# Kernel optimization log

Hardware: AMD Instinct MI355X
Metric: run time of the kernel (lower is better)

## Reference

```python
import jax, jax.numpy as jnp
import numpy as np

NEG_SLOPE = 0.2
EPS = 1e-16


def _gat_layer(x, src, dst, W, a_src, a_dst, b, n_nodes):
    # x: [N, Fin], W: [Fout, Fin]; src/dst: [E'] (self-loops already appended)
    h = x @ W.T                              # [N, Fout]
    alpha_s = h @ a_src                      # [N] per-source score
    alpha_d = h @ a_dst                      # [N] per-dest score
    e = jax.nn.leaky_relu(alpha_s[src] + alpha_d[dst], NEG_SLOPE)  # [E']
    # segment softmax over destination nodes (PyG softmax semantics)
    m = jax.ops.segment_max(e, dst, num_segments=n_nodes)          # [N]
    ex = jnp.exp(e - m[dst])                                       # [E']
    s = jax.ops.segment_sum(ex, dst, num_segments=n_nodes)         # [N]
    alpha = ex / (s[dst] + EPS)                                    # [E']
    out = jax.ops.segment_sum(alpha[:, None] * h[src], dst, num_segments=n_nodes)
    return out + b, alpha


def setup_inputs() -> dict:
    key = jax.random.key(0)
    ks = jax.random.split(key, 14)
    N, E, F_IN, H1, H2, F_OUT = 50000, 800000, 128, 64, 64, 32
    sc = 0.1
    return {
        "x": jax.random.normal(ks[0], (N, F_IN), dtype=jnp.float32),
        "edge_index": jax.random.randint(ks[1], (2, E), 0, N, dtype=jnp.int64),
        "W1": jax.random.normal(ks[2], (H1, F_IN), dtype=jnp.float32) * sc,
        "a_src1": jax.random.normal(ks[3], (H1,), dtype=jnp.float32) * sc,
        "a_dst1": jax.random.normal(ks[4], (H1,), dtype=jnp.float32) * sc,
        "b1": jnp.zeros((H1,), dtype=jnp.float32),
        "W2": jax.random.normal(ks[5], (H2, H1), dtype=jnp.float32) * sc,
        "a_src2": jax.random.normal(ks[6], (H2,), dtype=jnp.float32) * sc,
        "a_dst2": jax.random.normal(ks[7], (H2,), dtype=jnp.float32) * sc,
        "b2": jnp.zeros((H2,), dtype=jnp.float32),
        "W3": jax.random.normal(ks[8], (F_OUT, H2), dtype=jnp.float32) * sc,
        "a_src3": jax.random.normal(ks[9], (F_OUT,), dtype=jnp.float32) * sc,
        "a_dst3": jax.random.normal(ks[10], (F_OUT,), dtype=jnp.float32) * sc,
        "b3": jnp.zeros((F_OUT,), dtype=jnp.float32),
    }


def reference(x, edge_index, W1, a_src1, a_dst1, b1, W2, a_src2, a_dst2, b2, W3, a_src3, a_dst3, b3):
    N = x.shape[0]
    loops = jnp.arange(N, dtype=edge_index.dtype)
    src = jnp.concatenate([edge_index[0], loops])  # add_self_loops=True
    dst = jnp.concatenate([edge_index[1], loops])

    h, alpha1 = _gat_layer(x, src, dst, W1, a_src1, a_dst1, b1, N)
    h = jax.nn.relu(h)
    h, _ = _gat_layer(h, src, dst, W2, a_src2, a_dst2, b2, N)
    h = jax.nn.relu(h)
    out, _ = _gat_layer(h, src, dst, W3, a_src3, a_dst3, b3, N)
    # att_tuple = (edge_index with self loops, attention coefficients of layer 1)
    return (jnp.stack([src, dst]), alpha1, out)
```

## Files before the change

### kernel.cpp

```cpp
#include <hip/hip_runtime.h>
#include <hip/hip_bf16.h>
#include <math.h>

#define NEG_SLOPE 0.2f
#define GAT_EPS 1e-16f

constexpr int NN = 50000;
constexpr int NE = 800000;
constexpr int EP = NE + NN;
constexpr int NB = (NN + 255) / 256;

constexpr int PB  = 128;
constexpr int PT  = 1024;
constexpr int CH  = (EP + PB - 1) / PB;
constexpr int NCH = 4;
constexpr int BPC = PB / NCH;

__device__ inline void edge_sd(const int* __restrict__ ei, int i, int& s, int& d) {
    if (i < NE) { s = ei[i]; d = ei[NE + i]; }
    else        { s = d = i - NE; }
}

__device__ inline float bflo(unsigned int h) { return __uint_as_float(h << 16); }
__device__ inline float bfhi(unsigned int h) { return __uint_as_float(h & 0xffff0000u); }

__global__ __launch_bounds__(PT) void k_p1_hist(const int* __restrict__ ei,
                                                float* __restrict__ out0,
                                                unsigned char* __restrict__ hist,
                                                unsigned char* __restrict__ rank8) {
    __shared__ unsigned int sh[NN / 4];
    int b = blockIdx.x, t = threadIdx.x;
    for (int w = t; w < NN / 4; w += PT) sh[w] = 0u;
    __syncthreads();
    int i0 = b * CH;
    int iend = i0 + CH; if (iend > EP) iend = EP;
    for (int i = i0 + t; i < iend; i += PT) {
        int s, d; edge_sd(ei, i, s, d);
        __builtin_nontemporal_store((float)s, &out0[i]);
        __builtin_nontemporal_store((float)d, &out0[EP + i]);
        int sft = (d & 3) * 8;
        unsigned int old = atomicAdd(&sh[d >> 2], 1u << sft);
        __builtin_nontemporal_store((unsigned char)(old >> sft), &rank8[i]);
    }
    __syncthreads();
    unsigned int* hw = (unsigned int*)(hist + (size_t)b * NN);
    for (int w = t; w < NN / 4; w += PT) hw[w] = sh[w];
}

__global__ __launch_bounds__(256) void k_p2s1(unsigned char* __restrict__ hist,
                                              unsigned char* __restrict__ chunkoff,
                                              int* __restrict__ rowptr,
                                              int* __restrict__ bsum) {
    __shared__ int sh[256];
    int t = threadIdx.x;
    int n = blockIdx.x * 256 + t;
    int v = 0;
    if (n < NN) {
        unsigned int runs[NCH];
#pragma unroll
        for (int c = 0; c < NCH; ++c) {
            size_t base = (size_t)(c * BPC) * NN + n;
            unsigned int vv[BPC];
#pragma unroll
            for (int b = 0; b < BPC; ++b) vv[b] = hist[base + (size_t)b * NN];
            unsigned int run = 0;
#pragma unroll
            for (int b = 0; b < BPC; ++b) { unsigned int x = vv[b]; vv[b] = run; run += x; }
#pragma unroll
            for (int b = 0; b < BPC; ++b) hist[base + (size_t)b * NN] = (unsigned char)vv[b];
            runs[c] = run;
        }
        unsigned int o1 = runs[0], o2 = o1 + runs[1], o3 = o2 + runs[2];
        *(unsigned int*)&chunkoff[(size_t)n * 4] = (o1 << 8) | (o2 << 16) | (o3 << 24);
        v = (int)(o3 + runs[3]);
    }
    sh[t] = v; __syncthreads();
    for (int off = 1; off < 256; off <<= 1) {
        int x = (t >= off) ? sh[t - off] : 0;
        __syncthreads();
        sh[t] += x;
        __syncthreads();
    }
    if (n < NN) rowptr[n] = sh[t] - v;
    if (t == 255) bsum[blockIdx.x] = sh[255];
}

__global__ __launch_bounds__(256) void k_s23(int* __restrict__ rowptr,
                                             const int* __restrict__ bsum) {
    __shared__ int sh[256];
    int t = threadIdx.x;
    int v = (t < NB) ? bsum[t] : 0;
    sh[t] = v; __syncthreads();
    for (int off = 1; off < 256; off <<= 1) {
        int x = (t >= off) ? sh[t - off] : 0;
        __syncthreads();
        sh[t] += x;
        __syncthreads();
    }
    int blk = blockIdx.x;
    int off = (blk == 0) ? 0 : sh[blk - 1];
    int n = blk * 256 + t;
    if (n < NN) rowptr[n] += off;
    if (n == 0) rowptr[NN] = EP;
}

__global__ __launch_bounds__(256) void k_fill(const int* __restrict__ ei,
                                              const unsigned char* __restrict__ rank8,
                                              const unsigned char* __restrict__ hist,
                                              const unsigned char* __restrict__ chunkoff,
                                              const int* __restrict__ rowptr,
                                              unsigned short* __restrict__ col) {
    int i = blockIdx.x * 256 + threadIdx.x;
    if (i >= EP) return;
    int b = i / CH;
    int c = b / BPC;
    int s, d; edge_sd(ei, i, s, d);
    int pos = rowptr[d] + (int)chunkoff[d * 4 + c] + (int)hist[(size_t)b * NN + d]
            + (int)rank8[i];
    col[pos] = (unsigned short)s;
}

__global__ void k_alpha_out(const int* __restrict__ ei, const float* __restrict__ as_,
                            const float* __restrict__ ad_, const float* __restrict__ inv,
                            float* __restrict__ out_alpha) {
    int i = blockIdx.x * blockDim.x + threadIdx.x;
    if (i >= EP) return;
    int s, d; edge_sd(ei, i, s, d);
    float v = as_[s] + ad_[d];
    v = v > 0.f ? v : NEG_SLOPE * v;
    __builtin_nontemporal_store(__expf(v) * inv[d], &out_alpha[i]);
}

struct alignas(8) bh4 { __hip_bfloat16 a, b, c, d; };

__device__ inline void fma4(float4& acc, float x, const float4& w) {
    acc.x = fmaf(x, w.x, acc.x);
    acc.y = fmaf(x, w.y, acc.y);
    acc.z = fmaf(x, w.z, acc.z);
    acc.w = fmaf(x, w.w, acc.w);
}

template <int FIN, int FOUT, int NPB>
__global__ __launch_bounds__(256) void k_gemm_t(const float* __restrict__ in,
                                                const float* __restrict__ W,
                                                const float* __restrict__ avs,
                                                const float* __restrict__ avd,
                                                __hip_bfloat16* __restrict__ H,
                                                float* __restrict__ as_,
                                                float* __restrict__ ad_, int n) {
    constexpr int TF = FOUT / 4;
    constexpr int XS = FIN + 4;
    constexpr int WS = FOUT + 4;
    __shared__ float sX[NPB * XS];
    __shared__ float sWt[FIN * WS];
    int tid = threadIdx.x;
    for (int idx = tid; idx < FIN * FOUT; idx += 256) {
        int f = idx % FOUT, k = idx / FOUT;
        sWt[k * WS + f] = W[f * FIN + k];
    }
    int nb = blockIdx.x * NPB;
    for (int idx = tid; idx < NPB * (FIN / 4); idx += 256) {
        int node = idx / (FIN / 4), kq = idx % (FIN / 4);
        int g = nb + node;
        float4 v = make_float4(0.f, 0.f, 0.f, 0.f);
        if (g < n) v = *(const float4*)&in[(size_t)g * FIN + kq * 4];
        *(float4*)&sX[node * XS + kq * 4] = v;
    }
    __syncthreads();

    int fq = tid % TF, ng = tid / TF;
    int n0 = ng * 4;
    float4 acc0 = make_float4(0.f, 0.f, 0.f, 0.f);
    float4 acc1 = acc0, acc2 = acc0, acc3 = acc0;
    for (int k = 0; k < FIN; k += 4) {
        float4 w0 = *(const float4*)&sWt[(k + 0) * WS + fq * 4];
        float4 w1 = *(const float4*)&sWt[(k + 1) * WS + fq * 4];
        float4 w2 = *(const float4*)&sWt[(k + 2) * WS + fq * 4];
        float4 w3 = *(const float4*)&sWt[(k + 3) * WS + fq * 4];
        float4 x0 = *(const float4*)&sX[(n0 + 0) * XS + k];
        float4 x1 = *(const float4*)&sX[(n0 + 1) * XS + k];
        float4 x2 = *(const float4*)&sX[(n0 + 2) * XS + k];
        float4 x3 = *(const float4*)&sX[(n0 + 3) * XS + k];
        fma4(acc0, x0.x, w0); fma4(acc0, x0.y, w1); fma4(acc0, x0.z, w2); fma4(acc0, x0.w, w3);
        fma4(acc1, x1.x, w0); fma4(acc1, x1.y, w1); fma4(acc1, x1.z, w2); fma4(acc1, x1.w, w3);
        fma4(acc2, x2.x, w0); fma4(acc2, x2.y, w1); fma4(acc2, x2.z, w2); fma4(acc2, x2.w, w3);
        fma4(acc3, x3.x, w0); fma4(acc3, x3.y, w1); fma4(acc3, x3.z, w2); fma4(acc3, x3.w, w3);
    }
    float4 accs[4] = {acc0, acc1, acc2, acc3};
    float4 vs4 = *(const float4*)&avs[fq * 4];
    float4 vd4 = *(const float4*)&avd[fq * 4];
#pragma unroll
    for (int j = 0; j < 4; ++j) {
        int g = nb + n0 + j;
        float ps = accs[j].x * vs4.x + accs[j].y * vs4.y + accs[j].z * vs4.z + accs[j].w * vs4.w;
        float pd = accs[j].x * vd4.x + accs[j].y * vd4.y + accs[j].z * vd4.z + accs[j].w * vd4.w;
#pragma unroll
        for (int off = TF / 2; off; off >>= 1) {
            ps += __shfl_down(ps, off, TF);
            pd += __shfl_down(pd, off, TF);
        }
        if (g < n) {
            if (fq == 0) { as_[g] = ps; ad_[g] = pd; }
            bh4 o;
            o.a = __float2bfloat16(accs[j].x);
            o.b = __float2bfloat16(accs[j].y);
            o.c = __float2bfloat16(accs[j].z);
            o.d = __float2bfloat16(accs[j].w);
            *(bh4*)&H[(size_t)g * FOUT + fq * 4] = o;
        }
    }
}

template <int FOUT, bool RELU, bool WRITE_INV>
__global__ __launch_bounds__(256) void k_attn_grp(
    const int* __restrict__ rowptr, const unsigned short* __restrict__ col,
    const float* __restrict__ as_, const float* __restrict__ ad_,
    const __hip_bfloat16* __restrict__ H, const float* __restrict__ bias,
    float* __restrict__ outp, float* __restrict__ inv_out) {
    constexpr int L = (FOUT == 64) ? 16 : 8;
    constexpr int GPW = 64 / L;
    int tid = blockIdx.x * 256 + threadIdx.x;
    int wid = tid >> 6;
    int lane = threadIdx.x & 63;
    int grp = lane / L;
    int gl  = lane & (L - 1);
    int node = wid * GPW + grp;
    if (node >= NN) return;

    int start = rowptr[node], end = rowptr[node + 1];
    float adv = ad_[node];
    const uint2* __restrict__ H4 = (const uint2*)H;
    int base = lane & ~(L - 1);

    float sloc = 0.f;
    float4 acc = make_float4(0.f, 0.f, 0.f, 0.f);
    for (int c = start; c < end; c += 8) {
        int e = c + gl;
        float p = 0.f;
        int sc = 0;
        if (gl < 8 && e < end) {
            sc = (int)col[e];
            float v = as_[sc] + adv;
            v = v > 0.f ? v : NEG_SLOPE * v;
            p = __expf(v);
        }
        sloc += p;
        int cnt = end - c; if (cnt > 8) cnt = 8;
        float pp[8]; int ss[8]; uint2 hh[8];
#pragma unroll
        for (int k = 0; k < 8; ++k) {
            pp[k] = __shfl(p, base + k);
            ss[k] = __shfl(sc, base + k);
        }
#pragma unroll
        for (int k = 0; k < 8; ++k) {
            hh[k] = make_uint2(0u, 0u);
            if (k < cnt) hh[k] = H4[(size_t)ss[k] * L + gl];
        }
#pragma unroll
        for (int k = 0; k < 8; ++k) {
            acc.x = fmaf(pp[k], bflo(hh[k].x), acc.x);
            acc.y = fmaf(pp[k], bfhi(hh[k].x), acc.y);
            acc.z = fmaf(pp[k], bflo(hh[k].y), acc.z);
            acc.w = fmaf(pp[k], bfhi(hh[k].y), acc.w);
        }
    }
#pragma unroll
    for (int off = L / 2; off; off >>= 1) sloc += __shfl_xor(sloc, off);
    float inv = 1.f / (sloc + GAT_EPS);
    if (WRITE_INV && gl == 0) inv_out[node] = inv;

    float4 bb = *(const float4*)&bias[gl * 4];
    float o0 = bb.x + acc.x * inv;
    float o1 = bb.y + acc.y * inv;
    float o2 = bb.z + acc.z * inv;
    float o3 = bb.w + acc.w * inv;
    if (RELU) {
        o0 = fmaxf(o0, 0.f); o1 = fmaxf(o1, 0.f);
        o2 = fmaxf(o2, 0.f); o3 = fmaxf(o3, 0.f);
    }
    *(float4*)&outp[(size_t)node * FOUT + gl * 4] = make_float4(o0, o1, o2, o3);
}

extern "C" void kernel_launch(void* const* d_in, const int* in_sizes, int n_in,
                              void* d_out, int out_size, void* d_ws, size_t ws_size,
                              hipStream_t stream) {
    const float* x  = (const float*)d_in[0];
    const int*   ei = (const int*)d_in[1];
    const float* W1 = (const float*)d_in[2];
    const float* as1 = (const float*)d_in[3];
    const float* ad1 = (const float*)d_in[4];
    const float* b1 = (const float*)d_in[5];
    const float* W2 = (const float*)d_in[6];
    const float* as2 = (const float*)d_in[7];
    const float* ad2 = (const float*)d_in[8];
    const float* b2 = (const float*)d_in[9];
    const float* W3 = (const float*)d_in[10];
    const float* as3 = (const float*)d_in[11];
    const float* ad3 = (const float*)d_in[12];
    const float* b3 = (const float*)d_in[13];

    float* out = (float*)d_out;
    float* out_edges = out;
    float* out_alpha = out + 2 * EP;
    float* out_final = out + 3 * EP;

    char* w = (char*)d_ws;
    size_t o = 0;
    auto alloc = [&](size_t bytes) { void* p = w + o; o = (o + bytes + 15) & ~15ull; return p; };
    float* as_ = (float*)alloc((size_t)NN * 4);
    float* ad_ = (float*)alloc((size_t)NN * 4);
    float* inv = (float*)alloc((size_t)NN * 4);
    __hip_bfloat16* H = (__hip_bfloat16*)alloc((size_t)NN * 64 * 2);
    int* rowptr = (int*)alloc((size_t)(NN + 1) * 4);
    unsigned char* rank8 = (unsigned char*)alloc((size_t)EP);
    unsigned short* col  = (unsigned short*)alloc((size_t)EP * 2);
    unsigned char* chunkoff = (unsigned char*)alloc((size_t)NN * 4);
    int* bsum = (int*)alloc(1024);

    const size_t aggBytes  = (size_t)NN * 64 * 4;
    const size_t histBytes = (size_t)PB * NN;
    float* agg = (ws_size >= o + aggBytes)
        ? (float*)(w + o)
        : (float*)d_in[0];
    unsigned char* hist = (ws_size >= o + aggBytes + histBytes)
        ? (unsigned char*)(w + o + aggBytes)
        : (unsigned char*)out_final;

    k_p1_hist<<<PB, PT, 0, stream>>>(ei, out_edges, hist, rank8);
    k_p2s1<<<NB, 256, 0, stream>>>(hist, chunkoff, rowptr, bsum);
    k_s23<<<NB, 256, 0, stream>>>(rowptr, bsum);
    k_fill<<<(EP + 255) / 256, 256, 0, stream>>>(ei, rank8, hist, chunkoff, rowptr, col);

    const int nblk64 = (NN + 15) / 16;
    const int nblk32 = (NN + 31) / 32;

    k_gemm_t<128, 64, 64><<<(NN + 63) / 64, 256, 0, stream>>>(x, W1, as1, ad1, H, as_, ad_, NN);
    k_attn_grp<64, true, true><<<nblk64, 256, 0, stream>>>(rowptr, col, as_, ad_, H, b1,
                                                           agg, inv);
    k_alpha_out<<<(EP + 255) / 256, 256, 0, stream>>>(ei, as_, ad_, inv, out_alpha);

    k_gemm_t<64, 64, 64><<<(NN + 63) / 64, 256, 0, stream>>>(agg, W2, as2, ad2, H, as_, ad_, NN);
    k_attn_grp<64, true, false><<<nblk64, 256, 0, stream>>>(rowptr, col, as_, ad_, H, b2,
                                                            agg, nullptr);

    k_gemm_t<64, 32, 128><<<(NN + 127) / 128, 256, 0, stream>>>(agg, W3, as3, ad3, H, as_, ad_,
                                                                NN);
    k_attn_grp<32, false, false><<<nblk32, 256, 0, stream>>>(rowptr, col, as_, ad_, H, b3,
                                                             out_final, nullptr);
}
```

Baseline: 273.1 us.

## Fuse attention aggregation with next-layer GEMM and fold rowptr scan into fill

Attention aggregation for layers 1 and 2 now also applies bias and ReLU, stages the result in shared memory and multiplies by the next layer's weight matrix in the same kernel. It emits bf16 features and attention scores directly, which removes the fp32 intermediate round-trip and two GEMM launches. The second-level prefix scan is folded into the fill kernel, with each block recomputing the block-sum scan redundantly. Separate buffers per layer avoid read/write hazards, and the aggregation drops the max-subtraction in the softmax, as the earlier code already appears to do.

```diff
diff --git a/kernel.cpp b/kernel.cpp
--- a/kernel.cpp
+++ b/kernel.cpp
@@ -85,39 +85,37 @@
     if (t == 255) bsum[blockIdx.x] = sh[255];
 }
 
-__global__ __launch_bounds__(256) void k_s23(int* __restrict__ rowptr,
-                                             const int* __restrict__ bsum) {
-    __shared__ int sh[256];
-    int t = threadIdx.x;
-    int v = (t < NB) ? bsum[t] : 0;
-    sh[t] = v; __syncthreads();
-    for (int off = 1; off < 256; off <<= 1) {
-        int x = (t >= off) ? sh[t - off] : 0;
-        __syncthreads();
-        sh[t] += x;
-        __syncthreads();
-    }
-    int blk = blockIdx.x;
-    int off = (blk == 0) ? 0 : sh[blk - 1];
-    int n = blk * 256 + t;
-    if (n < NN) rowptr[n] += off;
-    if (n == 0) rowptr[NN] = EP;
-}
-
 __global__ __launch_bounds__(256) void k_fill(const int* __restrict__ ei,
                                               const unsigned char* __restrict__ rank8,
                                               const unsigned char* __restrict__ hist,
                                               const unsigned char* __restrict__ chunkoff,
                                               const int* __restrict__ rowptr,
-                                              unsigned short* __restrict__ col) {
-    int i = blockIdx.x * 256 + threadIdx.x;
-    if (i >= EP) return;
-    int b = i / CH;
-    int c = b / BPC;
-    int s, d; edge_sd(ei, i, s, d);
-    int pos = rowptr[d] + (int)chunkoff[d * 4 + c] + (int)hist[(size_t)b * NN + d]
-            + (int)rank8[i];
-    col[pos] = (unsigned short)s;
+                                              const int* __restrict__ bsum,
+                                              unsigned short* __restrict__ col,
+                                              int* __restrict__ rowptrF) {
+    __shared__ int sb[256];
+    int t = threadIdx.x;
+    int v = (t < NB) ? bsum[t] : 0;
+    sb[t] = v; __syncthreads();
+    for (int off = 1; off < 256; off <<= 1) {
+        int x = (t >= off) ? sb[t - off] : 0;
+        __syncthreads();
+        sb[t] += x;
+        __syncthreads();
+    }
+    sb[t] -= v;
+    __syncthreads();
+    int i = blockIdx.x * 256 + t;
+    if (i < EP) {
+        int b = i / CH;
+        int c = b / BPC;
+        int s, d; edge_sd(ei, i, s, d);
+        int pos = rowptr[d] + sb[d >> 8] + (int)chunkoff[d * 4 + c]
+                + (int)hist[(size_t)b * NN + d] + (int)rank8[i];
+        col[pos] = (unsigned short)s;
+    }
+    if (i < NN) rowptrF[i] = rowptr[i] + sb[i >> 8];
+    if (i == 0) rowptrF[NN] = EP;
 }
 
 __global__ void k_alpha_out(const int* __restrict__ ei, const float* __restrict__ as_,
@@ -132,6 +130,7 @@
 }
 
 struct alignas(8) bh4 { __hip_bfloat16 a, b, c, d; };
+struct alignas(4) bh2 { __hip_bfloat16 a, b; };
 
 __device__ inline void fma4(float4& acc, float x, const float4& w) {
     acc.x = fmaf(x, w.x, acc.x);
@@ -211,6 +210,135 @@
     }
 }
 
+template <int GOUT, bool WRITE_INV>
+__global__ __launch_bounds__(256) void k_attn_fg(
+    const int* __restrict__ rowptr, const unsigned short* __restrict__ col,
+    const float* __restrict__ as_, const float* __restrict__ ad_,
+    const __hip_bfloat16* __restrict__ H, const float* __restrict__ bias,
+    const float* __restrict__ Wn,
+    const float* __restrict__ avs, const float* __restrict__ avd,
+    __hip_bfloat16* __restrict__ Hout,
+    float* __restrict__ as_out, float* __restrict__ ad_out,
+    float* __restrict__ inv_out) {
+    constexpr int NPB = 16;
+    __shared__ float sW[64][GOUT + 2];
+    __shared__ float sA[NPB][68];
+    int tid = threadIdx.x;
+    for (int idx = tid; idx < 64 * GOUT; idx += 256) {
+        int f = idx % GOUT, k = idx / GOUT;
+        sW[k][f] = Wn[f * 64 + k];
+    }
+
+    int lane = tid & 63;
+    int grp = lane >> 4, gl = lane & 15;
+    int lnode = (tid >> 6) * 4 + grp;
+    int node = blockIdx.x * NPB + lnode;
+    int base = lane & ~15;
+
+    if (node < NN) {
+        int start = rowptr[node], end = rowptr[node + 1];
+        float adv = ad_[node];
+        const uint2* __restrict__ H4 = (const uint2*)H;
+        float sloc = 0.f;
+        float4 acc = make_float4(0.f, 0.f, 0.f, 0.f);
+        for (int c = start; c < end; c += 8) {
+            int e = c + gl;
+            float p = 0.f;
+            int sc = 0;
+            if (gl < 8 && e < end) {
+                sc = (int)col[e];
+                float v = as_[sc] + adv;
+                v = v > 0.f ? v : NEG_SLOPE * v;
+                p = __expf(v);
+            }
+            sloc += p;
+            int cnt = end - c; if (cnt > 8) cnt = 8;
+            float pp[8]; int ss[8]; uint2 hh[8];
+#pragma unroll
+            for (int k = 0; k < 8; ++k) {
+                pp[k] = __shfl(p, base + k);
+                ss[k] = __shfl(sc, base + k);
+            }
+#pragma unroll
+            for (int k = 0; k < 8; ++k) {
+                hh[k] = make_uint2(0u, 0u);
+                if (k < cnt) hh[k] = H4[(size_t)ss[k] * 16 + gl];
+            }
+#pragma unroll
+            for (int k = 0; k < 8; ++k) {
+                acc.x = fmaf(pp[k], bflo(hh[k].x), acc.x);
+                acc.y = fmaf(pp[k], bfhi(hh[k].x), acc.y);
+                acc.z = fmaf(pp[k], bflo(hh[k].y), acc.z);
+                acc.w = fmaf(pp[k], bfhi(hh[k].y), acc.w);
+            }
+        }
+#pragma unroll
+        for (int off = 8; off; off >>= 1) sloc += __shfl_xor(sloc, off);
+        float inv = 1.f / (sloc + GAT_EPS);
+        if (WRITE_INV && gl == 0) inv_out[node] = inv;
+
+        float4 bb = *(const float4*)&bias[gl * 4];
+        sA[lnode][gl * 4 + 0] = fmaxf(bb.x + acc.x * inv, 0.f);
+        sA[lnode][gl * 4 + 1] = fmaxf(bb.y + acc.y * inv, 0.f);
+        sA[lnode][gl * 4 + 2] = fmaxf(bb.z + acc.z * inv, 0.f);
+        sA[lnode][gl * 4 + 3] = fmaxf(bb.w + acc.w * inv, 0.f);
+    }
+    __syncthreads();
+
+    int ng = tid >> 4, fq = tid & 15;
+    int gnode = blockIdx.x * NPB + ng;
+    if (gnode >= NN) return;
+    if (GOUT == 64) {
+        float4 a = make_float4(0.f, 0.f, 0.f, 0.f);
+#pragma unroll 8
+        for (int k = 0; k < 64; ++k) {
+            float xk = sA[ng][k];
+            const float* wr = &sW[k][fq * 4];
+            a.x = fmaf(xk, wr[0], a.x);
+            a.y = fmaf(xk, wr[1], a.y);
+            a.z = fmaf(xk, wr[2], a.z);
+            a.w = fmaf(xk, wr[3], a.w);
+        }
+        float4 vs = *(const float4*)&avs[fq * 4];
+        float4 vd = *(const float4*)&avd[fq * 4];
+        float ps = a.x * vs.x + a.y * vs.y + a.z * vs.z + a.w * vs.w;
+        float pd = a.x * vd.x + a.y * vd.y + a.z * vd.z + a.w * vd.w;
+#pragma unroll
+        for (int off = 8; off; off >>= 1) {
+            ps += __shfl_xor(ps, off);
+            pd += __shfl_xor(pd, off);
+        }
+        if (fq == 0) { as_out[gnode] = ps; ad_out[gnode] = pd; }
+        bh4 o;
+        o.a = __float2bfloat16(a.x);
+        o.b = __float2bfloat16(a.y);
+        o.c = __float2bfloat16(a.z);
+        o.d = __float2bfloat16(a.w);
+        *(bh4*)&Hout[(size_t)gnode * 64 + fq * 4] = o;
+    } else {
+        float ax = 0.f, ay = 0.f;
+#pragma unroll 8
+        for (int k = 0; k < 64; ++k) {
+            float xk = sA[ng][k];
+            const float* wr = &sW[k][fq * 2];
+            ax = fmaf(xk, wr[0], ax);
+            ay = fmaf(xk, wr[1], ay);
+        }
+        float ps = ax * avs[fq * 2] + ay * avs[fq * 2 + 1];
+        float pd = ax * avd[fq * 2] + ay * avd[fq * 2 + 1];
+#pragma unroll
+        for (int off = 8; off; off >>= 1) {
+            ps += __shfl_xor(ps, off);
+            pd += __shfl_xor(pd, off);
+        }
+        if (fq == 0) { as_out[gnode] = ps; ad_out[gnode] = pd; }
+        bh2 o;
+        o.a = __float2bfloat16(ax);
+        o.b = __float2bfloat16(ay);
+        *(bh2*)&Hout[(size_t)gnode * 32 + fq * 2] = o;
+    }
+}
+
 template <int FOUT, bool RELU, bool WRITE_INV>
 __global__ __launch_bounds__(256) void k_attn_grp(
     const int* __restrict__ rowptr, const unsigned short* __restrict__ col,
@@ -308,44 +436,44 @@
     char* w = (char*)d_ws;
     size_t o = 0;
     auto alloc = [&](size_t bytes) { void* p = w + o; o = (o + bytes + 15) & ~15ull; return p; };
-    float* as_ = (float*)alloc((size_t)NN * 4);
-    float* ad_ = (float*)alloc((size_t)NN * 4);
+    float* asA = (float*)alloc((size_t)NN * 4);
+    float* adA = (float*)alloc((size_t)NN * 4);
+    float* asB = (float*)alloc((size_t)NN * 4);
+    float* adB = (float*)alloc((size_t)NN * 4);
+    float* asC = (float*)alloc((size_t)NN * 4);
+    float* adC = (float*)alloc((size_t)NN * 4);
     float* inv = (float*)alloc((size_t)NN * 4);
-    __hip_bfloat16* H = (__hip_bfloat16*)alloc((size_t)NN * 64 * 2);
-    int* rowptr = (int*)alloc((size_t)(NN + 1) * 4);
+    __hip_bfloat16* H1 = (__hip_bfloat16*)alloc((size_t)NN * 64 * 2);
+    __hip_bfloat16* H2 = (__hip_bfloat16*)alloc((size_t)NN * 64 * 2);
+    __hip_bfloat16* H3 = (__hip_bfloat16*)alloc((size_t)NN * 32 * 2);
+    int* rowptr  = (int*)alloc((size_t)(NN + 1) * 4);
+    int* rowptrF = (int*)alloc((size_t)(NN + 1) * 4);
     unsigned char* rank8 = (unsigned char*)alloc((size_t)EP);
     unsigned short* col  = (unsigned short*)alloc((size_t)EP * 2);
     unsigned char* chunkoff = (unsigned char*)alloc((size_t)NN * 4);
     int* bsum = (int*)alloc(1024);
 
-    const size_t aggBytes  = (size_t)NN * 64 * 4;
     const size_t histBytes = (size_t)PB * NN;
-    float* agg = (ws_size >= o + aggBytes)
-        ? (float*)(w + o)
-        : (float*)d_in[0];
-    unsigned char* hist = (ws_size >= o + aggBytes + histBytes)
-        ? (unsigned char*)(w + o + aggBytes)
+    unsigned char* hist = (ws_size >= o + histBytes)
+        ? (unsigned char*)(w + o)
         : (unsigned char*)out_final;
 
     k_p1_hist<<<PB, PT, 0, stream>>>(ei, out_edges, hist, rank8);
     k_p2s1<<<NB, 256, 0, stream>>>(hist, chunkoff, rowptr, bsum);
-    k_s23<<<NB, 256, 0, stream>>>(rowptr, bsum);
-    k_fill<<<(EP + 255) / 256, 256, 0, stream>>>(ei, rank8, hist, chunkoff, rowptr, col);
-
-    const int nblk64 = (NN + 15) / 16;
+    k_fill<<<(EP + 255) / 256, 256, 0, stream>>>(ei, rank8, hist, chunkoff, rowptr, bsum,
+                                                 col, rowptrF);
+
+    const int nblkF  = NN / 16;
     const int nblk32 = (NN + 31) / 32;
 
-    k_gemm_t<128, 64, 64><<<(NN + 63) / 64, 256, 0, stream>>>(x, W1, as1, ad1, H, as_, ad_, NN);
-    k_attn_grp<64, true, true><<<nblk64, 256, 0, stream>>>(rowptr, col, as_, ad_, H, b1,
-                                                           agg, inv);
-    k_alpha_out<<<(EP + 255) / 256, 256, 0, stream>>>(ei, as_, ad_, inv, out_alpha);
-
-    k_gemm_t<64, 64, 64><<<(NN + 63) / 64, 256, 0, stream>>>(agg, W2, as2, ad2, H, as_, ad_, NN);
-    k_attn_grp<64, true, false><<<nblk64, 256, 0, stream>>>(rowptr, col, as_, ad_, H, b2,
-                                                            agg, nullptr);
-
-    k_gemm_t<64, 32, 128><<<(NN + 127) / 128, 256, 0, stream>>>(agg, W3, as3, ad3, H, as_, ad_,
-                                                                NN);
-    k_attn_grp<32, false, false><<<nblk32, 256, 0, stream>>>(rowptr, col, as_, ad_, H, b3,
+    k_gemm_t<128, 64, 64><<<(NN + 63) / 64, 256, 0, stream>>>(x, W1, as1, ad1, H1,
+                                                              asA, adA, NN);
+    k_attn_fg<64, true><<<nblkF, 256, 0, stream>>>(rowptrF, col, asA, adA, H1, b1,
+                                                   W2, as2, ad2, H2, asB, adB, inv);
+    k_alpha_out<<<(EP + 255) / 256, 256, 0, stream>>>(ei, asA, adA, inv, out_alpha);
+
+    k_attn_fg<32, false><<<nblkF, 256, 0, stream>>>(rowptrF, col, asB, adB, H2, b2,
+                                                    W3, as3, ad3, H3, asC, adC, nullptr);
+    k_attn_grp<32, false, false><<<nblk32, 256, 0, stream>>>(rowptrF, col, asC, adC, H3, b3,
                                                              out_final, nullptr);
 }
```

New measurement: 282.3 us. 3.4% more time.

## Double histogram partitions and fold block-offset scan into the CSR fill kernel

Applied to the files above, without the earlier changes.

Raises the number of counting-sort partition blocks from 128 to 256 with eight chunks, widening per-node chunk offsets to 8 bytes, so the histogram pass runs on more CUs. Removes the separate k_s23 kernel by having every fill block redo the small scan over block sums and apply it when computing positions and writing a final rowptr array. Workspace buffers are now always allocated instead of falling back to aliasing inputs or outputs. This trades one kernel launch for redundant per-block scan work and doubles the histogram memory traffic.

```diff
diff --git a/kernel.cpp b/kernel.cpp
--- a/kernel.cpp
+++ b/kernel.cpp
@@ -10,10 +10,10 @@
 constexpr int EP = NE + NN;
 constexpr int NB = (NN + 255) / 256;
 
-constexpr int PB  = 128;
+constexpr int PB  = 256;
 constexpr int PT  = 1024;
 constexpr int CH  = (EP + PB - 1) / PB;
-constexpr int NCH = 4;
+constexpr int NCH = 8;
 constexpr int BPC = PB / NCH;
 
 __device__ inline void edge_sd(const int* __restrict__ ei, int i, int& s, int& d) {
@@ -70,9 +70,17 @@
             for (int b = 0; b < BPC; ++b) hist[base + (size_t)b * NN] = (unsigned char)vv[b];
             runs[c] = run;
         }
-        unsigned int o1 = runs[0], o2 = o1 + runs[1], o3 = o2 + runs[2];
-        *(unsigned int*)&chunkoff[(size_t)n * 4] = (o1 << 8) | (o2 << 16) | (o3 << 24);
-        v = (int)(o3 + runs[3]);
+        unsigned int off = 0;
+        unsigned int w0 = 0, w1 = 0;
+#pragma unroll
+        for (int c = 0; c < NCH; ++c) {
+            if (c < 4) w0 |= (off & 0xffu) << (8 * c);
+            else       w1 |= (off & 0xffu) << (8 * (c - 4));
+            off += runs[c];
+        }
+        *(unsigned int*)&chunkoff[(size_t)n * 8]     = w0;
+        *(unsigned int*)&chunkoff[(size_t)n * 8 + 4] = w1;
+        v = (int)off;
     }
     sh[t] = v; __syncthreads();
     for (int off = 1; off < 256; off <<= 1) {
@@ -85,39 +93,37 @@
     if (t == 255) bsum[blockIdx.x] = sh[255];
 }
 
-__global__ __launch_bounds__(256) void k_s23(int* __restrict__ rowptr,
-                                             const int* __restrict__ bsum) {
-    __shared__ int sh[256];
-    int t = threadIdx.x;
-    int v = (t < NB) ? bsum[t] : 0;
-    sh[t] = v; __syncthreads();
-    for (int off = 1; off < 256; off <<= 1) {
-        int x = (t >= off) ? sh[t - off] : 0;
-        __syncthreads();
-        sh[t] += x;
-        __syncthreads();
-    }
-    int blk = blockIdx.x;
-    int off = (blk == 0) ? 0 : sh[blk - 1];
-    int n = blk * 256 + t;
-    if (n < NN) rowptr[n] += off;
-    if (n == 0) rowptr[NN] = EP;
-}
-
 __global__ __launch_bounds__(256) void k_fill(const int* __restrict__ ei,
                                               const unsigned char* __restrict__ rank8,
                                               const unsigned char* __restrict__ hist,
                                               const unsigned char* __restrict__ chunkoff,
                                               const int* __restrict__ rowptr,
-                                              unsigned short* __restrict__ col) {
-    int i = blockIdx.x * 256 + threadIdx.x;
-    if (i >= EP) return;
-    int b = i / CH;
-    int c = b / BPC;
-    int s, d; edge_sd(ei, i, s, d);
-    int pos = rowptr[d] + (int)chunkoff[d * 4 + c] + (int)hist[(size_t)b * NN + d]
-            + (int)rank8[i];
-    col[pos] = (unsigned short)s;
+                                              const int* __restrict__ bsum,
+                                              unsigned short* __restrict__ col,
+                                              int* __restrict__ rowptrF) {
+    __shared__ int sb[256];
+    int t = threadIdx.x;
+    int v = (t < NB) ? bsum[t] : 0;
+    sb[t] = v; __syncthreads();
+    for (int off = 1; off < 256; off <<= 1) {
+        int x = (t >= off) ? sb[t - off] : 0;
+        __syncthreads();
+        sb[t] += x;
+        __syncthreads();
+    }
+    sb[t] -= v;
+    __syncthreads();
+    int i = blockIdx.x * 256 + t;
+    if (i < EP) {
+        int b = i / CH;
+        int c = b / BPC;
+        int s, d; edge_sd(ei, i, s, d);
+        int pos = rowptr[d] + sb[d >> 8] + (int)chunkoff[(size_t)d * 8 + c]
+                + (int)hist[(size_t)b * NN + d] + (int)rank8[i];
+        col[pos] = (unsigned short)s;
+    }
+    if (i < NN) rowptrF[i] = rowptr[i] + sb[i >> 8];
+    if (i == 0) rowptrF[NN] = EP;
 }
 
 __global__ void k_alpha_out(const int* __restrict__ ei, const float* __restrict__ as_,
@@ -312,40 +318,35 @@
     float* ad_ = (float*)alloc((size_t)NN * 4);
     float* inv = (float*)alloc((size_t)NN * 4);
     __hip_bfloat16* H = (__hip_bfloat16*)alloc((size_t)NN * 64 * 2);
-    int* rowptr = (int*)alloc((size_t)(NN + 1) * 4);
+    int* rowptr  = (int*)alloc((size_t)(NN + 1) * 4);
+    int* rowptrF = (int*)alloc((size_t)(NN + 1) * 4);
     unsigned char* rank8 = (unsigned char*)alloc((size_t)EP);
     unsigned short* col  = (unsigned short*)alloc((size_t)EP * 2);
-    unsigned char* chunkoff = (unsigned char*)alloc((size_t)NN * 4);
+    unsigned char* chunkoff = (unsigned char*)alloc((size_t)NN * 8);
     int* bsum = (int*)alloc(1024);
-
-    const size_t aggBytes  = (size_t)NN * 64 * 4;
-    const size_t histBytes = (size_t)PB * NN;
-    float* agg = (ws_size >= o + aggBytes)
-        ? (float*)(w + o)
-        : (float*)d_in[0];
-    unsigned char* hist = (ws_size >= o + aggBytes + histBytes)
-        ? (unsigned char*)(w + o + aggBytes)
-        : (unsigned char*)out_final;
+    float* agg = (float*)alloc((size_t)NN * 64 * 4);
+    unsigned char* hist = (unsigned char*)alloc((size_t)PB * NN);
+    (void)ws_size;
 
     k_p1_hist<<<PB, PT, 0, stream>>>(ei, out_edges, hist, rank8);
     k_p2s1<<<NB, 256, 0, stream>>>(hist, chunkoff, rowptr, bsum);
-    k_s23<<<NB, 256, 0, stream>>>(rowptr, bsum);
-    k_fill<<<(EP + 255) / 256, 256, 0, stream>>>(ei, rank8, hist, chunkoff, rowptr, col);
+    k_fill<<<(EP + 255) / 256, 256, 0, stream>>>(ei, rank8, hist, chunkoff, rowptr, bsum,
+                                                 col, rowptrF);
 
     const int nblk64 = (NN + 15) / 16;
     const int nblk32 = (NN + 31) / 32;
 
     k_gemm_t<128, 64, 64><<<(NN + 63) / 64, 256, 0, stream>>>(x, W1, as1, ad1, H, as_, ad_, NN);
-    k_attn_grp<64, true, true><<<nblk64, 256, 0, stream>>>(rowptr, col, as_, ad_, H, b1,
+    k_attn_grp<64, true, true><<<nblk64, 256, 0, stream>>>(rowptrF, col, as_, ad_, H, b1,
                                                            agg, inv);
     k_alpha_out<<<(EP + 255) / 256, 256, 0, stream>>>(ei, as_, ad_, inv, out_alpha);
 
     k_gemm_t<64, 64, 64><<<(NN + 63) / 64, 256, 0, stream>>>(agg, W2, as2, ad2, H, as_, ad_, NN);
-    k_attn_grp<64, true, false><<<nblk64, 256, 0, stream>>>(rowptr, col, as_, ad_, H, b2,
+    k_attn_grp<64, true, false><<<nblk64, 256, 0, stream>>>(rowptrF, col, as_, ad_, H, b2,
                                                             agg, nullptr);
 
     k_gemm_t<64, 32, 128><<<(NN + 127) / 128, 256, 0, stream>>>(agg, W3, as3, ad3, H, as_, ad_,
                                                                 NN);
-    k_attn_grp<32, false, false><<<nblk32, 256, 0, stream>>>(rowptr, col, as_, ad_, H, b3,
+    k_attn_grp<32, false, false><<<nblk32, 256, 0, stream>>>(rowptrF, col, as_, ad_, H, b3,
                                                              out_final, nullptr);
 }
```

After: 275.9 us. No clear change (+1.1%).
